# Performance work log

Measured on AMD Instinct MI355X. Metric: run time of the kernel, lower is better.

Reference implementation:

```python
import jax, jax.numpy as jnp
import numpy as np

N_NODES = 50000
N_EDGES = 800000
IN_DIM = 128
HID = 32
HEADS = 4
OUT_DIM = 2
NEG_SLOPE = 0.2


def gat_conv(feat, W, al, ar, bias, src, dst, n_nodes):
    """DGL GATConv (eval mode, no dropout). feat: [N, Fin]; W: [Fin, H*D];
    al, ar: [H, D]; bias: [H*D]. Returns [N, H, D]."""
    H, D = al.shape
    hf = (feat @ W).reshape(n_nodes, H, D)              # [N,H,D]
    el = jnp.einsum('nhd,hd->nh', hf, al)               # [N,H]
    er = jnp.einsum('nhd,hd->nh', hf, ar)               # [N,H]
    e = el[src] + er[dst]                               # [E,H]
    e = jax.nn.leaky_relu(e, NEG_SLOPE)
    # segment softmax over incoming edges of each dst node
    emax = jax.ops.segment_max(e, dst, num_segments=n_nodes)  # [N,H]
    emax = jnp.where(jnp.isfinite(emax), emax, 0.0)
    ex = jnp.exp(e - emax[dst])                         # [E,H]
    denom = jax.ops.segment_sum(ex, dst, num_segments=n_nodes)  # [N,H]
    alpha = ex / jnp.maximum(denom[dst], 1e-30)         # [E,H]
    msg = hf[src] * alpha[:, :, None]                   # [E,H,D]
    out = jax.ops.segment_sum(msg, dst, num_segments=n_nodes)   # [N,H,D]
    return out + bias.reshape(1, H, D)


def setup_inputs() -> dict:
    key = jax.random.key(0)
    ks = jax.random.split(key, 16)
    f32 = jnp.float32
    in_feat = jax.random.normal(ks[0], (N_NODES, IN_DIM), dtype=f32)
    src = jax.random.randint(ks[1], (N_EDGES,), 0, N_NODES)
    dst = jax.random.randint(ks[2], (N_EDGES,), 0, N_NODES)
    s1 = 1.0 / np.sqrt(IN_DIM)
    s2 = 1.0 / np.sqrt(HID * HEADS)
    W1 = jax.random.normal(ks[3], (IN_DIM, HEADS * HID), dtype=f32) * s1
    al1 = jax.random.normal(ks[4], (HEADS, HID), dtype=f32) * 0.1
    ar1 = jax.random.normal(ks[5], (HEADS, HID), dtype=f32) * 0.1
    b1 = jnp.zeros((HEADS * HID,), dtype=f32)
    W2 = jax.random.normal(ks[6], (HEADS * HID, HEADS * HID), dtype=f32) * s2
    al2 = jax.random.normal(ks[7], (HEADS, HID), dtype=f32) * 0.1
    ar2 = jax.random.normal(ks[8], (HEADS, HID), dtype=f32) * 0.1
    b2 = jnp.zeros((HEADS * HID,), dtype=f32)
    Wout = jax.random.normal(ks[9], (HID, OUT_DIM), dtype=f32) * (1.0 / np.sqrt(HID))
    bout = jnp.zeros((OUT_DIM,), dtype=f32)
    return {"in_feat": in_feat, "W1": W1, "al1": al1, "ar1": ar1, "b1": b1,
            "W2": W2, "al2": al2, "ar2": ar2, "b2": b2,
            "Wout": Wout, "bout": bout, "src": src, "dst": dst}


def reference(in_feat, W1, al1, ar1, b1, W2, al2, ar2, b2, Wout, bout, src, dst):
    h = gat_conv(in_feat, W1, al1, ar1, b1, src, dst, N_NODES)  # [N,H,D]
    h = jax.nn.relu(h.reshape(N_NODES, HEADS * HID))            # flatten(1) + relu
    h = gat_conv(h, W2, al2, ar2, b2, src, dst, N_NODES)        # [N,H,D]
    emd = h.mean(axis=1)                                        # mean over heads -> [N,D]
    logits = jax.nn.relu(emd) @ Wout + bout                     # [N,2]
    return jax.nn.softmax(logits, axis=-1)
```

## Files before the change

kernel.cpp:

```cpp
#include <hip/hip_runtime.h>
#include <cmath>

#define N_NODES 50000
#define N_EDGES 800000
#define NBUCK 196
#define NHB 196
#define EPB 4096

typedef unsigned short u16;
typedef unsigned int u32;
typedef __attribute__((ext_vector_type(8))) short bf16x8;
typedef __attribute__((ext_vector_type(4))) float f32x4;

static __device__ __forceinline__ float lrelu(float x) { return x > 0.f ? x : 0.2f * x; }
static __device__ __forceinline__ float bf2f(u16 u) { return __uint_as_float(((u32)u) << 16); }
static __device__ __forceinline__ float bflo(u32 u) { return __uint_as_float(u << 16); }
static __device__ __forceinline__ float bfhi(u32 u) { return __uint_as_float(u & 0xFFFF0000u); }
static __device__ __forceinline__ u16 f2bf(float f) {
    u32 b = __float_as_uint(f);
    return (u16)((b + 0x7FFFu + ((b >> 16) & 1u)) >> 16);
}
static __device__ __forceinline__ u32 pack2(float a, float b) {
    return (u32)f2bf(a) | ((u32)f2bf(b) << 16);
}

__global__ __launch_bounds__(1024) void bhist_k(const int* __restrict__ dst, u32* __restrict__ bcnt) {
    __shared__ u32 hist[NBUCK];
    int tid = threadIdx.x;
    for (int i = tid; i < NBUCK; i += 1024) hist[i] = 0;
    __syncthreads();
    int base = blockIdx.x * EPB;
#pragma unroll
    for (int k = 0; k < 4; ++k) {
        int e = base + k * 1024 + tid;
        if (e < N_EDGES) atomicAdd(&hist[dst[e] >> 8], 1u);
    }
    __syncthreads();
    for (int i = tid; i < NBUCK; i += 1024) bcnt[(size_t)blockIdx.x * NBUCK + i] = hist[i];
}

__global__ __launch_bounds__(256) void bscan_k(const u32* __restrict__ bcnt, u32* __restrict__ wbase,
                                               int* __restrict__ bstart) {
    __shared__ int s[256];
    int t = threadIdx.x;
    u32 run = 0;
    if (t < NBUCK) {
        for (int blk = 0; blk < NHB; ++blk) {
            u32 v = bcnt[(size_t)blk * NBUCK + t];
            wbase[(size_t)blk * NBUCK + t] = run;
            run += v;
        }
    }
    s[t] = (t < NBUCK) ? (int)run : 0;
    __syncthreads();
    for (int o = 1; o < 256; o <<= 1) {
        int v = (t >= o) ? s[t - o] : 0;
        __syncthreads();
        s[t] += v;
        __syncthreads();
    }
    if (t < NBUCK) bstart[t] = (t == 0) ? 0 : s[t - 1];
    if (t == NBUCK - 1) bstart[NBUCK] = s[t];
}

__global__ __launch_bounds__(1024) void bscatter_k(const int* __restrict__ src, const int* __restrict__ dst,
                                                   const u32* __restrict__ wbase, const int* __restrict__ bstart,
                                                   u32* __restrict__ bucketed) {
    __shared__ u32 pos[NBUCK];
    int tid = threadIdx.x;
    for (int i = tid; i < NBUCK; i += 1024)
        pos[i] = (u32)bstart[i] + wbase[(size_t)blockIdx.x * NBUCK + i];
    __syncthreads();
    int base = blockIdx.x * EPB;
#pragma unroll
    for (int k = 0; k < 4; ++k) {
        int e = base + k * 1024 + tid;
        if (e < N_EDGES) {
            int d = dst[e];
            int b = d >> 8;
            u32 p = atomicAdd(&pos[b], 1u);
            bucketed[p] = (u32)src[e] | ((u32)(d & 255) << 16);
        }
    }
}

__global__ __launch_bounds__(256) void bcsr_k(const u32* __restrict__ bucketed, const int* __restrict__ bstart,
                                              int* __restrict__ offs, u16* __restrict__ srcs) {
    __shared__ u32 cnt[256];
    __shared__ int s[256];
    __shared__ u32 fp[256];
    int b = blockIdx.x;
    int tid = threadIdx.x;
    int ebeg = bstart[b], eend = bstart[b + 1];
    int ne = eend - ebeg;
    cnt[tid] = 0;
    __syncthreads();
    for (int i = tid; i < ne; i += 256)
        atomicAdd(&cnt[bucketed[ebeg + i] >> 16], 1u);
    __syncthreads();
    s[tid] = (int)cnt[tid];
    __syncthreads();
    for (int o = 1; o < 256; o <<= 1) {
        int v = (tid >= o) ? s[tid - o] : 0;
        __syncthreads();
        s[tid] += v;
        __syncthreads();
    }
    int excl = s[tid] - (int)cnt[tid];
    int node = b * 256 + tid;
    if (node < N_NODES) offs[node] = ebeg + excl;
    if (b == NBUCK - 1 && tid == 0) offs[N_NODES] = N_EDGES;
    fp[tid] = (u32)excl;
    __syncthreads();
    for (int i = tid; i < ne; i += 256) {
        u32 u = bucketed[ebeg + i];
        u32 p = atomicAdd(&fp[u >> 16], 1u);
        srcs[ebeg + p] = (u16)(u & 0xFFFFu);
    }
}

__global__ __launch_bounds__(256) void packW_k(const float* __restrict__ W, u16* __restrict__ Wp) {
    int i = blockIdx.x * 256 + threadIdx.x;
    if (i >= 16384) return;
    int j = i & 7, lane = (i >> 3) & 63, ks = (i >> 9) & 3, nt = i >> 11;
    int k = ks * 32 + (lane >> 4) * 8 + j;
    int ncol = nt * 16 + (lane & 15);
    Wp[i] = f2bf(W[k * 128 + ncol]);
}

template <int BF16IN>
__global__ __launch_bounds__(256) void gemm_mfma(
    const void* __restrict__ Xv, const u16* __restrict__ Wp,
    const float* __restrict__ al, const float* __restrict__ ar,
    u16* __restrict__ hf, float* __restrict__ el, float* __restrict__ er, int n)
{
    __shared__ u16 xs[64][136];
    int row0 = blockIdx.x * 64;
    int tid = threadIdx.x;
    if (BF16IN) {
        const uint4* Xb = (const uint4*)Xv;
        for (int i = tid; i < 1024; i += 256) {
            int r = i >> 4, c = i & 15;
            uint4 v = make_uint4(0u, 0u, 0u, 0u);
            if (row0 + r < n) v = Xb[(size_t)(row0 + r) * 16 + c];
            ((uint4*)&xs[r][0])[c] = v;
        }
    } else {
        const float4* X4 = (const float4*)Xv;
        for (int i = tid; i < 2048; i += 256) {
            int r = i >> 5, c = i & 31;
            float4 v = make_float4(0.f, 0.f, 0.f, 0.f);
            if (row0 + r < n) v = X4[(size_t)(row0 + r) * 32 + c];
            ((uint2*)&xs[r][0])[c] = make_uint2(pack2(v.x, v.y), pack2(v.z, v.w));
        }
    }
    __syncthreads();

    int wave = tid >> 6, lane = tid & 63;
    int quad = lane >> 4, l15 = lane & 15;

    bf16x8 bfrag[2][4];
#pragma unroll
    for (int ct = 0; ct < 2; ++ct) {
        int nt = wave * 2 + ct;
#pragma unroll
        for (int ks = 0; ks < 4; ++ks)
            bfrag[ct][ks] = *(const bf16x8*)(Wp + ((((nt * 4 + ks) * 64) + lane) << 3));
    }

    f32x4 acc[4][2];
#pragma unroll
    for (int rt = 0; rt < 4; ++rt)
#pragma unroll
        for (int ct = 0; ct < 2; ++ct)
            acc[rt][ct] = (f32x4){0.f, 0.f, 0.f, 0.f};

#pragma unroll
    for (int ks = 0; ks < 4; ++ks) {
#pragma unroll
        for (int rt = 0; rt < 4; ++rt) {
            bf16x8 a = *(const bf16x8*)&xs[rt * 16 + l15][ks * 32 + quad * 8];
            acc[rt][0] = __builtin_amdgcn_mfma_f32_16x16x32_bf16(a, bfrag[0][ks], acc[rt][0], 0, 0, 0);
            acc[rt][1] = __builtin_amdgcn_mfma_f32_16x16x32_bf16(a, bfrag[1][ks], acc[rt][1], 0, 0, 0);
        }
    }

    float alv0 = al[wave * 32 + l15], alv1 = al[wave * 32 + 16 + l15];
    float arv0 = ar[wave * 32 + l15], arv1 = ar[wave * 32 + 16 + l15];
#pragma unroll
    for (int rt = 0; rt < 4; ++rt) {
#pragma unroll
        for (int r = 0; r < 4; ++r) {
            int row = row0 + rt * 16 + quad * 4 + r;
            float c0 = acc[rt][0][r], c1 = acc[rt][1][r];
            if (row < n) {
                hf[(size_t)row * 128 + wave * 32 + l15] = f2bf(c0);
                hf[(size_t)row * 128 + wave * 32 + 16 + l15] = f2bf(c1);
            }
            float pel = c0 * alv0 + c1 * alv1;
            float per = c0 * arv0 + c1 * arv1;
            pel += __shfl_xor(pel, 1); pel += __shfl_xor(pel, 2);
            pel += __shfl_xor(pel, 4); pel += __shfl_xor(pel, 8);
            per += __shfl_xor(per, 1); per += __shfl_xor(per, 2);
            per += __shfl_xor(per, 4); per += __shfl_xor(per, 8);
            if (l15 == 0 && row < n) {
                el[row * 4 + wave] = pel;
                er[row * 4 + wave] = per;
            }
        }
    }
}

static __device__ __forceinline__ void agg_core(
    int node, int lane, const int* __restrict__ offs, const u16* __restrict__ srcs,
    const float* __restrict__ el, const float* __restrict__ er, const u16* __restrict__ hf,
    float acc[8], float& den)
{
    int qw = lane >> 4;
    int q = lane & 15;
    int h = q >> 2;
    float erh = er[node * 4 + h];
    int beg = offs[node], end = offs[node + 1];
    den = 0.f;
#pragma unroll
    for (int i = 0; i < 8; i++) acc[i] = 0.f;
    int base = beg;
    for (; base + 8 <= end; base += 8) {
        int s0 = srcs[base + qw];
        int s1 = srcs[base + 4 + qw];
        float w0 = __expf(lrelu(el[s0 * 4 + h] + erh));
        float w1 = __expf(lrelu(el[s1 * 4 + h] + erh));
        uint4 u0 = *(const uint4*)(hf + (size_t)s0 * 128 + q * 8);
        uint4 u1 = *(const uint4*)(hf + (size_t)s1 * 128 + q * 8);
        den += w0 + w1;
        acc[0] += w0 * bflo(u0.x) + w1 * bflo(u1.x);
        acc[1] += w0 * bfhi(u0.x) + w1 * bfhi(u1.x);
        acc[2] += w0 * bflo(u0.y) + w1 * bflo(u1.y);
        acc[3] += w0 * bfhi(u0.y) + w1 * bfhi(u1.y);
        acc[4] += w0 * bflo(u0.z) + w1 * bflo(u1.z);
        acc[5] += w0 * bfhi(u0.z) + w1 * bfhi(u1.z);
        acc[6] += w0 * bflo(u0.w) + w1 * bflo(u1.w);
        acc[7] += w0 * bfhi(u0.w) + w1 * bfhi(u1.w);
    }
    for (; base < end; base += 4) {
        int e = base + qw;
        bool valid = e < end;
        int ec = valid ? e : end - 1;
        int s = srcs[ec];
        float w = valid ? __expf(lrelu(el[s * 4 + h] + erh)) : 0.f;
        uint4 u = *(const uint4*)(hf + (size_t)s * 128 + q * 8);
        den += w;
        acc[0] += w * bflo(u.x);
        acc[1] += w * bfhi(u.x);
        acc[2] += w * bflo(u.y);
        acc[3] += w * bfhi(u.y);
        acc[4] += w * bflo(u.z);
        acc[5] += w * bfhi(u.z);
        acc[6] += w * bflo(u.w);
        acc[7] += w * bfhi(u.w);
    }
#pragma unroll
    for (int i = 0; i < 8; i++) {
        acc[i] += __shfl_xor(acc[i], 16);
        acc[i] += __shfl_xor(acc[i], 32);
    }
    den += __shfl_xor(den, 16);
    den += __shfl_xor(den, 32);
}

__global__ __launch_bounds__(256) void agg1_k(const int* __restrict__ offs, const u16* __restrict__ srcs,
                                              const float* __restrict__ el, const float* __restrict__ er,
                                              const u16* __restrict__ hf, const float* __restrict__ bias,
                                              u16* __restrict__ h1) {
    int node = blockIdx.x * 4 + (threadIdx.x >> 6);
    int lane = threadIdx.x & 63;
    if (node >= N_NODES) return;
    float acc[8], den;
    agg_core(node, lane, offs, srcs, el, er, hf, acc, den);
    int qw = lane >> 4, q = lane & 15;
    if (qw == 0) {
        float inv = 1.0f / fmaxf(den, 1e-30f);
        float o[8];
#pragma unroll
        for (int i = 0; i < 8; i++)
            o[i] = fmaxf(acc[i] * inv + bias[q * 8 + i], 0.f);
        uint4 pk;
        pk.x = pack2(o[0], o[1]);
        pk.y = pack2(o[2], o[3]);
        pk.z = pack2(o[4], o[5]);
        pk.w = pack2(o[6], o[7]);
        *(uint4*)(h1 + (size_t)node * 128 + q * 8) = pk;
    }
}

__global__ __launch_bounds__(256) void agg2_k(const int* __restrict__ offs, const u16* __restrict__ srcs,
                                              const float* __restrict__ el, const float* __restrict__ er,
                                              const u16* __restrict__ hf, const float* __restrict__ bias,
                                              const float* __restrict__ Wout, const float* __restrict__ bout,
                                              float2* __restrict__ out) {
    int node = blockIdx.x * 4 + (threadIdx.x >> 6);
    int lane = threadIdx.x & 63;
    if (node >= N_NODES) return;
    float acc[8], den;
    agg_core(node, lane, offs, srcs, el, er, hf, acc, den);
    int q = lane & 15;
    float inv = 1.0f / fmaxf(den, 1e-30f);
    float o[8];
#pragma unroll
    for (int i = 0; i < 8; i++) o[i] = acc[i] * inv + bias[q * 8 + i];
#pragma unroll
    for (int i = 0; i < 8; i++) {
        o[i] += __shfl_xor(o[i], 4);
        o[i] += __shfl_xor(o[i], 8);
        o[i] = fmaxf(0.25f * o[i], 0.f);
    }
    int d0 = (q & 3) * 8;
    float l0 = 0.f, l1 = 0.f;
#pragma unroll
    for (int i = 0; i < 8; i++) {
        l0 += o[i] * Wout[(d0 + i) * 2];
        l1 += o[i] * Wout[(d0 + i) * 2 + 1];
    }
    l0 += __shfl_xor(l0, 1); l0 += __shfl_xor(l0, 2);
    l1 += __shfl_xor(l1, 1); l1 += __shfl_xor(l1, 2);
    if (lane == 0) {
        l0 += bout[0];
        l1 += bout[1];
        float mx = fmaxf(l0, l1);
        float e0 = __expf(l0 - mx), e1 = __expf(l1 - mx);
        float invs = 1.f / (e0 + e1);
        out[node] = make_float2(e0 * invs, e1 * invs);
    }
}

extern "C" void kernel_launch(void* const* d_in, const int* in_sizes, int n_in,
                              void* d_out, int out_size, void* d_ws, size_t ws_size,
                              hipStream_t stream) {
    const float* in_feat = (const float*)d_in[0];
    const float* W1   = (const float*)d_in[1];
    const float* al1  = (const float*)d_in[2];
    const float* ar1  = (const float*)d_in[3];
    const float* b1   = (const float*)d_in[4];
    const float* W2   = (const float*)d_in[5];
    const float* al2  = (const float*)d_in[6];
    const float* ar2  = (const float*)d_in[7];
    const float* b2   = (const float*)d_in[8];
    const float* Wout = (const float*)d_in[9];
    const float* bout = (const float*)d_in[10];
    const int*   src  = (const int*)d_in[11];
    const int*   dst  = (const int*)d_in[12];
    float* out = (float*)d_out;

    char* ws = (char*)d_ws;
    size_t off = 0;
    auto carve = [&](size_t bytes) {
        char* p = ws + off;
        off = (off + bytes + 255) & ~(size_t)255;
        return p;
    };
    u16*   hfA      = (u16*)carve((size_t)N_NODES * 128 * 2);
    u16*   h1       = (u16*)carve((size_t)N_NODES * 128 * 2);
    float* el       = (float*)carve((size_t)N_NODES * 4 * 4);
    float* er       = (float*)carve((size_t)N_NODES * 4 * 4);
    u16*   srcs     = (u16*)carve((size_t)N_EDGES * 2);
    u32*   bucketed = (u32*)carve((size_t)N_EDGES * 4);
    u32*   bcnt     = (u32*)carve((size_t)NHB * NBUCK * 4);
    u32*   wbase    = (u32*)carve((size_t)NHB * NBUCK * 4);
    int*   bstart   = (int*)carve((size_t)(NBUCK + 1) * 4);
    int*   offs     = (int*)carve((size_t)(N_NODES + 1) * 4);
    u16*   Wp1      = (u16*)carve((size_t)16384 * 2);
    u16*   Wp2      = (u16*)carve((size_t)16384 * 2);
    (void)ws_size; (void)in_sizes; (void)n_in; (void)out_size;

    const int GB = (N_NODES + 63) / 64;
    const int AB = (N_NODES + 3) / 4;

    bhist_k<<<NHB, 1024, 0, stream>>>(dst, bcnt);
    packW_k<<<64, 256, 0, stream>>>(W1, Wp1);
    packW_k<<<64, 256, 0, stream>>>(W2, Wp2);
    bscan_k<<<1, 256, 0, stream>>>(bcnt, wbase, bstart);
    bscatter_k<<<NHB, 1024, 0, stream>>>(src, dst, wbase, bstart, bucketed);
    bcsr_k<<<NBUCK, 256, 0, stream>>>(bucketed, bstart, offs, srcs);

    gemm_mfma<0><<<GB, 256, 0, stream>>>(in_feat, Wp1, al1, ar1, hfA, el, er, N_NODES);
    agg1_k<<<AB, 256, 0, stream>>>(offs, srcs, el, er, hfA, b1, h1);

    gemm_mfma<1><<<GB, 256, 0, stream>>>(h1, Wp2, al2, ar2, hfA, el, er, N_NODES);
    agg2_k<<<AB, 256, 0, stream>>>(offs, srcs, el, er, hfA, b2, Wout, bout, (float2*)out);
}
```

Before: 226.3 us.

## Split node features into per-head planes and aggregate one head per block

```diff
diff --git a/kernel.cpp b/kernel.cpp
--- a/kernel.cpp
+++ b/kernel.cpp
@@ -6,6 +6,7 @@
 #define NBUCK 196
 #define NHB 196
 #define EPB 4096
+#define NBH 12500
 
 typedef unsigned short u16;
 typedef unsigned int u32;
@@ -119,9 +120,12 @@
     }
 }
 
-__global__ __launch_bounds__(256) void packW_k(const float* __restrict__ W, u16* __restrict__ Wp) {
-    int i = blockIdx.x * 256 + threadIdx.x;
-    if (i >= 16384) return;
+__global__ __launch_bounds__(256) void packW_k(const float* __restrict__ W1, const float* __restrict__ W2,
+                                               u16* __restrict__ Wp1, u16* __restrict__ Wp2) {
+    int gi = blockIdx.x * 256 + threadIdx.x;
+    const float* W = (gi < 16384) ? W1 : W2;
+    u16* Wp = (gi < 16384) ? Wp1 : Wp2;
+    int i = gi & 16383;
     int j = i & 7, lane = (i >> 3) & 63, ks = (i >> 9) & 3, nt = i >> 11;
     int k = ks * 32 + (lane >> 4) * 8 + j;
     int ncol = nt * 16 + (lane & 15);
@@ -132,7 +136,7 @@
 __global__ __launch_bounds__(256) void gemm_mfma(
     const void* __restrict__ Xv, const u16* __restrict__ Wp,
     const float* __restrict__ al, const float* __restrict__ ar,
-    u16* __restrict__ hf, float* __restrict__ el, float* __restrict__ er, int n)
+    u16* __restrict__ hfh, float* __restrict__ elh, float* __restrict__ erh, int n)
 {
     __shared__ u16 xs[64][136];
     int row0 = blockIdx.x * 64;
@@ -187,6 +191,7 @@
 
     float alv0 = al[wave * 32 + l15], alv1 = al[wave * 32 + 16 + l15];
     float arv0 = ar[wave * 32 + l15], arv1 = ar[wave * 32 + 16 + l15];
+    u16* hf_plane = hfh + (size_t)wave * N_NODES * 32;
 #pragma unroll
     for (int rt = 0; rt < 4; ++rt) {
 #pragma unroll
@@ -194,8 +199,8 @@
             int row = row0 + rt * 16 + quad * 4 + r;
             float c0 = acc[rt][0][r], c1 = acc[rt][1][r];
             if (row < n) {
-                hf[(size_t)row * 128 + wave * 32 + l15] = f2bf(c0);
-                hf[(size_t)row * 128 + wave * 32 + 16 + l15] = f2bf(c1);
+                hf_plane[(size_t)row * 32 + l15] = f2bf(c0);
+                hf_plane[(size_t)row * 32 + 16 + l15] = f2bf(c1);
             }
             float pel = c0 * alv0 + c1 * alv1;
             float per = c0 * arv0 + c1 * arv1;
@@ -204,132 +209,127 @@
             per += __shfl_xor(per, 1); per += __shfl_xor(per, 2);
             per += __shfl_xor(per, 4); per += __shfl_xor(per, 8);
             if (l15 == 0 && row < n) {
-                el[row * 4 + wave] = pel;
-                er[row * 4 + wave] = per;
+                elh[wave * N_NODES + row] = pel;
+                erh[wave * N_NODES + row] = per;
             }
         }
     }
 }
 
-static __device__ __forceinline__ void agg_core(
-    int node, int lane, const int* __restrict__ offs, const u16* __restrict__ srcs,
-    const float* __restrict__ el, const float* __restrict__ er, const u16* __restrict__ hf,
-    float acc[8], float& den)
-{
+template <int RELU>
+__global__ __launch_bounds__(256) void aggh_k(const int* __restrict__ offs, const u16* __restrict__ srcs,
+                                              const float* __restrict__ elh, const float* __restrict__ erh,
+                                              const u16* __restrict__ hfh, const float* __restrict__ bias,
+                                              u16* __restrict__ out) {
+    int head = blockIdx.x / NBH;
+    int ng = blockIdx.x - head * NBH;
+    int wave = threadIdx.x >> 6;
+    int node = ng * 4 + wave;
+    int lane = threadIdx.x & 63;
+    if (node >= N_NODES) return;
     int qw = lane >> 4;
     int q = lane & 15;
-    int h = q >> 2;
-    float erh = er[node * 4 + h];
+    const float* el = elh + (size_t)head * N_NODES;
+    const u32* hf32 = (const u32*)(hfh + (size_t)head * N_NODES * 32);
+    float erv = erh[(size_t)head * N_NODES + node];
     int beg = offs[node], end = offs[node + 1];
-    den = 0.f;
-#pragma unroll
-    for (int i = 0; i < 8; i++) acc[i] = 0.f;
-    int base = beg;
-    for (; base + 8 <= end; base += 8) {
-        int s0 = srcs[base + qw];
-        int s1 = srcs[base + 4 + qw];
-        float w0 = __expf(lrelu(el[s0 * 4 + h] + erh));
-        float w1 = __expf(lrelu(el[s1 * 4 + h] + erh));
-        uint4 u0 = *(const uint4*)(hf + (size_t)s0 * 128 + q * 8);
-        uint4 u1 = *(const uint4*)(hf + (size_t)s1 * 128 + q * 8);
-        den += w0 + w1;
-        acc[0] += w0 * bflo(u0.x) + w1 * bflo(u1.x);
-        acc[1] += w0 * bfhi(u0.x) + w1 * bfhi(u1.x);
-        acc[2] += w0 * bflo(u0.y) + w1 * bflo(u1.y);
-        acc[3] += w0 * bfhi(u0.y) + w1 * bfhi(u1.y);
-        acc[4] += w0 * bflo(u0.z) + w1 * bflo(u1.z);
-        acc[5] += w0 * bfhi(u0.z) + w1 * bfhi(u1.z);
-        acc[6] += w0 * bflo(u0.w) + w1 * bflo(u1.w);
-        acc[7] += w0 * bfhi(u0.w) + w1 * bfhi(u1.w);
-    }
-    for (; base < end; base += 4) {
-        int e = base + qw;
-        bool valid = e < end;
-        int ec = valid ? e : end - 1;
-        int s = srcs[ec];
-        float w = valid ? __expf(lrelu(el[s * 4 + h] + erh)) : 0.f;
-        uint4 u = *(const uint4*)(hf + (size_t)s * 128 + q * 8);
-        den += w;
-        acc[0] += w * bflo(u.x);
-        acc[1] += w * bfhi(u.x);
-        acc[2] += w * bflo(u.y);
-        acc[3] += w * bfhi(u.y);
-        acc[4] += w * bflo(u.z);
-        acc[5] += w * bfhi(u.z);
-        acc[6] += w * bflo(u.w);
-        acc[7] += w * bfhi(u.w);
-    }
-#pragma unroll
-    for (int i = 0; i < 8; i++) {
-        acc[i] += __shfl_xor(acc[i], 16);
-        acc[i] += __shfl_xor(acc[i], 32);
-    }
-    den += __shfl_xor(den, 16);
-    den += __shfl_xor(den, 32);
-}
-
-__global__ __launch_bounds__(256) void agg1_k(const int* __restrict__ offs, const u16* __restrict__ srcs,
-                                              const float* __restrict__ el, const float* __restrict__ er,
-                                              const u16* __restrict__ hf, const float* __restrict__ bias,
-                                              u16* __restrict__ h1) {
-    int node = blockIdx.x * 4 + (threadIdx.x >> 6);
-    int lane = threadIdx.x & 63;
-    if (node >= N_NODES) return;
-    float acc[8], den;
-    agg_core(node, lane, offs, srcs, el, er, hf, acc, den);
-    int qw = lane >> 4, q = lane & 15;
+    int deg = end - beg;
+    float a0 = 0.f, a1 = 0.f, den = 0.f;
+
+    if (deg <= 64) {
+        int psrc = (lane < deg) ? (int)srcs[beg + lane] : 0;
+        int base = beg;
+        for (; base + 16 <= end; base += 16) {
+            int j = base - beg + qw;
+            int s0 = __shfl(psrc, j);
+            int s1 = __shfl(psrc, j + 4);
+            int s2 = __shfl(psrc, j + 8);
+            int s3 = __shfl(psrc, j + 12);
+            float e0 = el[s0], e1 = el[s1], e2 = el[s2], e3 = el[s3];
+            u32 u0 = hf32[(size_t)s0 * 16 + q];
+            u32 u1 = hf32[(size_t)s1 * 16 + q];
+            u32 u2 = hf32[(size_t)s2 * 16 + q];
+            u32 u3 = hf32[(size_t)s3 * 16 + q];
+            float w0 = __expf(lrelu(e0 + erv));
+            float w1 = __expf(lrelu(e1 + erv));
+            float w2 = __expf(lrelu(e2 + erv));
+            float w3 = __expf(lrelu(e3 + erv));
+            den += (w0 + w1) + (w2 + w3);
+            a0 += w0 * bflo(u0) + w1 * bflo(u1) + w2 * bflo(u2) + w3 * bflo(u3);
+            a1 += w0 * bfhi(u0) + w1 * bfhi(u1) + w2 * bfhi(u2) + w3 * bfhi(u3);
+        }
+        for (; base + 8 <= end; base += 8) {
+            int j = base - beg + qw;
+            int s0 = __shfl(psrc, j);
+            int s1 = __shfl(psrc, j + 4);
+            float e0 = el[s0], e1 = el[s1];
+            u32 u0 = hf32[(size_t)s0 * 16 + q];
+            u32 u1 = hf32[(size_t)s1 * 16 + q];
+            float w0 = __expf(lrelu(e0 + erv));
+            float w1 = __expf(lrelu(e1 + erv));
+            den += w0 + w1;
+            a0 += w0 * bflo(u0) + w1 * bflo(u1);
+            a1 += w0 * bfhi(u0) + w1 * bfhi(u1);
+        }
+        for (; base < end; base += 4) {
+            int e = base + qw;
+            bool valid = e < end;
+            int j = valid ? (e - beg) : 0;
+            int s = __shfl(psrc, j);
+            float w = valid ? __expf(lrelu(el[s] + erv)) : 0.f;
+            u32 u = hf32[(size_t)s * 16 + q];
+            den += w;
+            a0 += w * bflo(u);
+            a1 += w * bfhi(u);
+        }
+    } else {
+        for (int base = beg; base < end; base += 4) {
+            int e = base + qw;
+            bool valid = e < end;
+            int ec = valid ? e : end - 1;
+            int s = srcs[ec];
+            float w = valid ? __expf(lrelu(el[s] + erv)) : 0.f;
+            u32 u = hf32[(size_t)s * 16 + q];
+            den += w;
+            a0 += w * bflo(u);
+            a1 += w * bfhi(u);
+        }
+    }
+    a0 += __shfl_xor(a0, 16); a0 += __shfl_xor(a0, 32);
+    a1 += __shfl_xor(a1, 16); a1 += __shfl_xor(a1, 32);
+    den += __shfl_xor(den, 16); den += __shfl_xor(den, 32);
     if (qw == 0) {
         float inv = 1.0f / fmaxf(den, 1e-30f);
-        float o[8];
-#pragma unroll
-        for (int i = 0; i < 8; i++)
-            o[i] = fmaxf(acc[i] * inv + bias[q * 8 + i], 0.f);
-        uint4 pk;
-        pk.x = pack2(o[0], o[1]);
-        pk.y = pack2(o[2], o[3]);
-        pk.z = pack2(o[4], o[5]);
-        pk.w = pack2(o[6], o[7]);
-        *(uint4*)(h1 + (size_t)node * 128 + q * 8) = pk;
-    }
-}
-
-__global__ __launch_bounds__(256) void agg2_k(const int* __restrict__ offs, const u16* __restrict__ srcs,
-                                              const float* __restrict__ el, const float* __restrict__ er,
-                                              const u16* __restrict__ hf, const float* __restrict__ bias,
-                                              const float* __restrict__ Wout, const float* __restrict__ bout,
-                                              float2* __restrict__ out) {
-    int node = blockIdx.x * 4 + (threadIdx.x >> 6);
-    int lane = threadIdx.x & 63;
+        float o0 = a0 * inv + bias[head * 32 + q * 2];
+        float o1 = a1 * inv + bias[head * 32 + q * 2 + 1];
+        if (RELU) { o0 = fmaxf(o0, 0.f); o1 = fmaxf(o1, 0.f); }
+        ((u32*)out)[(size_t)node * 64 + head * 16 + q] = pack2(o0, o1);
+    }
+}
+
+__global__ __launch_bounds__(256) void final_k(const u16* __restrict__ h2, const float* __restrict__ Wout,
+                                               const float* __restrict__ bout, float2* __restrict__ out) {
+    int tid = threadIdx.x;
+    int node = blockIdx.x * 8 + (tid >> 5);
+    int d = tid & 31;
     if (node >= N_NODES) return;
-    float acc[8], den;
-    agg_core(node, lane, offs, srcs, el, er, hf, acc, den);
-    int q = lane & 15;
-    float inv = 1.0f / fmaxf(den, 1e-30f);
-    float o[8];
-#pragma unroll
-    for (int i = 0; i < 8; i++) o[i] = acc[i] * inv + bias[q * 8 + i];
-#pragma unroll
-    for (int i = 0; i < 8; i++) {
-        o[i] += __shfl_xor(o[i], 4);
-        o[i] += __shfl_xor(o[i], 8);
-        o[i] = fmaxf(0.25f * o[i], 0.f);
-    }
-    int d0 = (q & 3) * 8;
-    float l0 = 0.f, l1 = 0.f;
-#pragma unroll
-    for (int i = 0; i < 8; i++) {
-        l0 += o[i] * Wout[(d0 + i) * 2];
-        l1 += o[i] * Wout[(d0 + i) * 2 + 1];
-    }
-    l0 += __shfl_xor(l0, 1); l0 += __shfl_xor(l0, 2);
-    l1 += __shfl_xor(l1, 1); l1 += __shfl_xor(l1, 2);
-    if (lane == 0) {
+    const u16* row = h2 + (size_t)node * 128;
+    float m = 0.25f * (bf2f(row[d]) + bf2f(row[32 + d]) + bf2f(row[64 + d]) + bf2f(row[96 + d]));
+    float r = fmaxf(m, 0.f);
+    float l0 = r * Wout[d * 2];
+    float l1 = r * Wout[d * 2 + 1];
+#pragma unroll
+    for (int off = 16; off; off >>= 1) {
+        l0 += __shfl_xor(l0, off, 32);
+        l1 += __shfl_xor(l1, off, 32);
+    }
+    if (d == 0) {
         l0 += bout[0];
         l1 += bout[1];
         float mx = fmaxf(l0, l1);
         float e0 = __expf(l0 - mx), e1 = __expf(l1 - mx);
-        float invs = 1.f / (e0 + e1);
-        out[node] = make_float2(e0 * invs, e1 * invs);
+        float inv = 1.f / (e0 + e1);
+        out[node] = make_float2(e0 * inv, e1 * inv);
     }
 }
 
@@ -358,10 +358,10 @@
         off = (off + bytes + 255) & ~(size_t)255;
         return p;
     };
-    u16*   hfA      = (u16*)carve((size_t)N_NODES * 128 * 2);
+    u16*   hfh      = (u16*)carve((size_t)N_NODES * 128 * 2);
     u16*   h1       = (u16*)carve((size_t)N_NODES * 128 * 2);
-    float* el       = (float*)carve((size_t)N_NODES * 4 * 4);
-    float* er       = (float*)carve((size_t)N_NODES * 4 * 4);
+    float* elh      = (float*)carve((size_t)N_NODES * 4 * 4);
+    float* erh      = (float*)carve((size_t)N_NODES * 4 * 4);
     u16*   srcs     = (u16*)carve((size_t)N_EDGES * 2);
     u32*   bucketed = (u32*)carve((size_t)N_EDGES * 4);
     u32*   bcnt     = (u32*)carve((size_t)NHB * NBUCK * 4);
@@ -373,18 +373,19 @@
     (void)ws_size; (void)in_sizes; (void)n_in; (void)out_size;
 
     const int GB = (N_NODES + 63) / 64;
-    const int AB = (N_NODES + 3) / 4;
+    const int FB = (N_NODES + 7) / 8;
 
     bhist_k<<<NHB, 1024, 0, stream>>>(dst, bcnt);
-    packW_k<<<64, 256, 0, stream>>>(W1, Wp1);
-    packW_k<<<64, 256, 0, stream>>>(W2, Wp2);
+    packW_k<<<128, 256, 0, stream>>>(W1, W2, Wp1, Wp2);
     bscan_k<<<1, 256, 0, stream>>>(bcnt, wbase, bstart);
     bscatter_k<<<NHB, 1024, 0, stream>>>(src, dst, wbase, bstart, bucketed);
     bcsr_k<<<NBUCK, 256, 0, stream>>>(bucketed, bstart, offs, srcs);
 
-    gemm_mfma<0><<<GB, 256, 0, stream>>>(in_feat, Wp1, al1, ar1, hfA, el, er, N_NODES);
-    agg1_k<<<AB, 256, 0, stream>>>(offs, srcs, el, er, hfA, b1, h1);
-
-    gemm_mfma<1><<<GB, 256, 0, stream>>>(h1, Wp2, al2, ar2, hfA, el, er, N_NODES);
-    agg2_k<<<AB, 256, 0, stream>>>(offs, srcs, el, er, hfA, b2, Wout, bout, (float2*)out);
-}
+    gemm_mfma<0><<<GB, 256, 0, stream>>>(in_feat, Wp1, al1, ar1, hfh, elh, erh, N_NODES);
+    aggh_k<1><<<4 * NBH, 256, 0, stream>>>(offs, srcs, elh, erh, hfh, b1, h1);
+
+    gemm_mfma<1><<<GB, 256, 0, stream>>>(h1, Wp2, al2, ar2, hfh, elh, erh, N_NODES);
+    aggh_k<0><<<4 * NBH, 256, 0, stream>>>(offs, srcs, elh, erh, hfh, b2, h1);
+
+    final_k<<<FB, 256, 0, stream>>>(h1, Wout, bout, (float2*)out);
+}
```

Result: slower. 312.2 us (+38.0%).
